# Performance work log

Measured on AMD Instinct MI355X. Metric: run time of the kernel, lower is better.

The kernel has to match this reference:

```python
import jax, jax.numpy as jnp
import numpy as np

B, T, I, H = 64, 2048, 64, 128


def setup_inputs() -> dict:
    key = jax.random.key(0)
    ks = jax.random.split(key, 6)
    std = 1.0 / np.sqrt(H)
    return {
        "x": jax.random.normal(ks[0], (B, T, I), dtype=jnp.float32),
        "h0": jax.random.normal(ks[1], (B, H), dtype=jnp.float32),
        "W": jax.random.uniform(ks[2], (H, I), dtype=jnp.float32, minval=-std, maxval=std),
        "U": jax.random.uniform(ks[3], (H, H), dtype=jnp.float32, minval=-std, maxval=std),
        "b_ih": jax.random.uniform(ks[4], (H,), dtype=jnp.float32, minval=-std, maxval=std),
        "b_hh": jax.random.uniform(ks[5], (H,), dtype=jnp.float32, minval=-std, maxval=std),
    }


def reference(x, h0, W, U, b_ih, b_hh):
    # Precompute the input projection for all timesteps in one big GEMM:
    # xw[b,t,h] = W x_t + b_ih + b_hh  (biases folded in once)
    xw = jnp.einsum("bti,hi->bth", x, W) + b_ih + b_hh  # [B,T,H]
    xw_t = jnp.swapaxes(xw, 0, 1)  # [T,B,H] for scan over time

    def step(h, xt):
        # vanilla tanh RNN cell: h' = tanh(W x + U h + b_ih + b_hh)
        h_new = jnp.tanh(xt + h @ U.T)
        return h_new, h_new

    h_last, ys = jax.lax.scan(step, h0, xw_t)  # ys: [T,B,H]
    output = jnp.swapaxes(ys, 0, 1)  # batch_first -> [B,T,H]
    return output, h_last
```

## Files before the change

### kernel.cpp

```cpp
#include <hip/hip_runtime.h>
#include <hip/hip_bf16.h>


#define RNN_B 64
#define RNN_T 2048
#define RNN_I 64
#define RNN_H 128
#define CH    32
#define NCH   (RNN_T / CH)

__device__ __forceinline__ float fast_tanh(float x) {
  float e = __builtin_amdgcn_exp2f(x * 2.885390081777927f);
  return 1.0f - 2.0f * __builtin_amdgcn_rcpf(e + 1.0f);
}

template <int CTRL>
__device__ __forceinline__ float dpp_add(float s) {
  int o = __builtin_amdgcn_mov_dpp(__float_as_int(s), CTRL, 0xF, 0xF, true);
  return s + __int_as_float(o);
}

__global__ __launch_bounds__(256) void rnn_xw_gemm(
    const float* __restrict__ x, const float* __restrict__ W,
    const float* __restrict__ b_ih, const float* __restrict__ b_hh,
    float* __restrict__ xw) {
  const int tid  = threadIdx.x;
  const int h    = tid >> 1;
  const int half = tid & 1;

  const float4* W4 = (const float4*)(W + h * RNN_I + half * 32);
  float4 w[8];
#pragma unroll
  for (int j = 0; j < 8; ++j) w[j] = W4[j];
  const float bias = b_ih[h] + b_hh[h];

  __shared__ __align__(16) float4 xs[64 * 16];
  const long rbase = (long)blockIdx.x * 64;
  const float4* xg = (const float4*)(x + rbase * RNN_I);
#pragma unroll
  for (int j = 0; j < 4; ++j) xs[tid + 256 * j] = xg[tid + 256 * j];
  __syncthreads();

  for (int r = 0; r < 64; ++r) {
    const float4* xr = xs + r * 16 + half * 8;
    float4 a = make_float4(0.f, 0.f, 0.f, 0.f);
#pragma unroll
    for (int j = 0; j < 8; ++j) {
      float4 xv = xr[j];
      a.x = fmaf(w[j].x, xv.x, a.x);
      a.y = fmaf(w[j].y, xv.y, a.y);
      a.z = fmaf(w[j].z, xv.z, a.z);
      a.w = fmaf(w[j].w, xv.w, a.w);
    }
    float s = (a.x + a.y) + (a.z + a.w);
    s = dpp_add<0xB1>(s);
    if (half == 0)
      xw[(rbase + r) * RNN_H + h] = s + bias;
  }
}

__global__ __launch_bounds__(512, 2) void rnn_scan(
    const float* xw,
    float* out, float* __restrict__ hlast,
    const float* __restrict__ h0, const float* __restrict__ U) {
  const int b   = blockIdx.x;
  const int tid = threadIdx.x;
  const int h   = tid >> 2;
  const int q   = tid & 3;

  __shared__ __align__(16) float hbuf[2][4 * 36];
  __shared__ __align__(16) float xbuf[CH * RNN_H];
  __shared__ __align__(16) float obuf[CH * RNN_H];

  const float4* U4 = (const float4*)(U + h * RNN_H + q * 32);
  float4 u[8];
#pragma unroll
  for (int j = 0; j < 8; ++j) u[j] = U4[j];

  if (tid < RNN_H) hbuf[0][(tid >> 5) * 36 + (tid & 31)] = h0[b * RNN_H + tid];

  const long base    = (long)b * RNN_T * RNN_H;
  const float4* xw4  = (const float4*)(xw + base);
  float4* out4       = (float4*)(out + base);
  float4* xb4        = (float4*)xbuf;
  const float4* ob4  = (const float4*)obuf;

  int cur = 0;
  for (int c = 0; c < NCH; ++c) {
    float4 xr0 = xw4[(long)c * 1024 + tid];
    float4 xr1 = xw4[(long)c * 1024 + tid + 512];
    if (c > 0) {
      float4 o0 = ob4[tid];
      float4 o1 = ob4[tid + 512];
      out4[(long)(c - 1) * 1024 + tid]       = o0;
      out4[(long)(c - 1) * 1024 + tid + 512] = o1;
    }
    xb4[tid]       = xr0;
    xb4[tid + 512] = xr1;
    __syncthreads();

    for (int tc = 0; tc < CH; ++tc) {
      const float4* hp = (const float4*)(hbuf[cur] + q * 36);
      float4 a = make_float4(0.f, 0.f, 0.f, 0.f);
#pragma unroll
      for (int j = 0; j < 8; ++j) {
        float4 hv = hp[j];
        a.x = fmaf(u[j].x, hv.x, a.x);
        a.y = fmaf(u[j].y, hv.y, a.y);
        a.z = fmaf(u[j].z, hv.z, a.z);
        a.w = fmaf(u[j].w, hv.w, a.w);
      }
      float s = (a.x + a.y) + (a.z + a.w);
      s = dpp_add<0xB1>(s);
      s = dpp_add<0x4E>(s);
      float val = fast_tanh(s + xbuf[tc * RNN_H + h]);
      if (q == 0) hbuf[cur ^ 1][(h >> 5) * 36 + (h & 31)] = val;
      if (q == 1) obuf[tc * RNN_H + h] = val;
      cur ^= 1;
      __syncthreads();
    }
  }

  out4[(long)(NCH - 1) * 1024 + tid]       = ob4[tid];
  out4[(long)(NCH - 1) * 1024 + tid + 512] = ob4[tid + 512];
  if (tid < RNN_H)
    hlast[b * RNN_H + tid] = hbuf[cur][(tid >> 5) * 36 + (tid & 31)];
}

extern "C" void kernel_launch(void* const* d_in, const int* in_sizes, int n_in,
                              void* d_out, int out_size, void* d_ws, size_t ws_size,
                              hipStream_t stream) {
  const float* x    = (const float*)d_in[0];
  const float* h0   = (const float*)d_in[1];
  const float* W    = (const float*)d_in[2];
  const float* U    = (const float*)d_in[3];
  const float* b_ih = (const float*)d_in[4];
  const float* b_hh = (const float*)d_in[5];

  float* out   = (float*)d_out;
  float* hlast = out + (long)RNN_B * RNN_T * RNN_H;

  rnn_xw_gemm<<<(RNN_B * RNN_T) / 64, 256, 0, stream>>>(x, W, b_ih, b_hh, out);
  rnn_scan<<<RNN_B, 512, 0, stream>>>(out, out, hlast, h0, U);
}
```

Measured before the change: 771.1 us.

## Register-tile 4 rows per thread in scan and GEMM, halve scan block size

After: 759.6 us. About the same (-1.5%).

```diff
diff --git a/kernel.cpp b/kernel.cpp
--- a/kernel.cpp
+++ b/kernel.cpp
@@ -1,5 +1,4 @@
 #include <hip/hip_runtime.h>
-#include <hip/hip_bf16.h>
 
 
 #define RNN_B 64
@@ -20,111 +19,150 @@
   return s + __int_as_float(o);
 }
 
-__global__ __launch_bounds__(256) void rnn_xw_gemm(
+__device__ __forceinline__ void fma4(float4& a, const float4 u, const float4 h) {
+  a.x = fmaf(u.x, h.x, a.x);
+  a.y = fmaf(u.y, h.y, a.y);
+  a.z = fmaf(u.z, h.z, a.z);
+  a.w = fmaf(u.w, h.w, a.w);
+}
+
+__device__ __forceinline__ float hsum(const float4 a) {
+  return (a.x + a.y) + (a.z + a.w);
+}
+
+__global__ __launch_bounds__(256, 2) void rnn_xw_gemm(
     const float* __restrict__ x, const float* __restrict__ W,
     const float* __restrict__ b_ih, const float* __restrict__ b_hh,
     float* __restrict__ xw) {
-  const int tid  = threadIdx.x;
-  const int h    = tid >> 1;
-  const int half = tid & 1;
+  const int tid   = threadIdx.x;
+  const int wave  = tid >> 6;
+  const int lane  = tid & 63;
+  const int whalf = wave & 1;
+  const int pair  = wave >> 1;
+  const int g2    = lane >> 2;
+  const int q2    = lane & 3;
 
-  const float4* W4 = (const float4*)(W + h * RNN_I + half * 32);
-  float4 w[8];
+  float4 w[4][4];
 #pragma unroll
-  for (int j = 0; j < 8; ++j) w[j] = W4[j];
-  const float bias = b_ih[h] + b_hh[h];
+  for (int r = 0; r < 4; ++r) {
+    const float4* Wr =
+        (const float4*)(W + (64 * whalf + 4 * g2 + r) * RNN_I + 16 * q2);
+#pragma unroll
+    for (int m = 0; m < 4; ++m) w[r][m] = Wr[m];
+  }
+  const int row_own = 64 * whalf + lane;
+  const float bias  = b_ih[row_own] + b_hh[row_own];
 
   __shared__ __align__(16) float4 xs[64 * 16];
   const long rbase = (long)blockIdx.x * 64;
   const float4* xg = (const float4*)(x + rbase * RNN_I);
 #pragma unroll
-  for (int j = 0; j < 4; ++j) xs[tid + 256 * j] = xg[tid + 256 * j];
+  for (int jj = 0; jj < 4; ++jj) xs[tid + 256 * jj] = xg[tid + 256 * jj];
   __syncthreads();
 
-  for (int r = 0; r < 64; ++r) {
-    const float4* xr = xs + r * 16 + half * 8;
-    float4 a = make_float4(0.f, 0.f, 0.f, 0.f);
+  for (int i = 0; i < 32; ++i) {
+    const int r = 32 * pair + i;
+    const float4* xr = xs + r * 16 + q2 * 4;
+    float4 a0 = {0,0,0,0}, a1 = {0,0,0,0}, a2 = {0,0,0,0}, a3 = {0,0,0,0};
 #pragma unroll
-    for (int j = 0; j < 8; ++j) {
-      float4 xv = xr[j];
-      a.x = fmaf(w[j].x, xv.x, a.x);
-      a.y = fmaf(w[j].y, xv.y, a.y);
-      a.z = fmaf(w[j].z, xv.z, a.z);
-      a.w = fmaf(w[j].w, xv.w, a.w);
+    for (int m = 0; m < 4; ++m) {
+      const float4 xv = xr[m];
+      fma4(a0, w[0][m], xv);
+      fma4(a1, w[1][m], xv);
+      fma4(a2, w[2][m], xv);
+      fma4(a3, w[3][m], xv);
     }
-    float s = (a.x + a.y) + (a.z + a.w);
-    s = dpp_add<0xB1>(s);
-    if (half == 0)
-      xw[(rbase + r) * RNN_H + h] = s + bias;
+    float s0 = hsum(a0), s1 = hsum(a1), s2 = hsum(a2), s3 = hsum(a3);
+    s0 = dpp_add<0xB1>(s0); s0 = dpp_add<0x4E>(s0);
+    s1 = dpp_add<0xB1>(s1); s1 = dpp_add<0x4E>(s1);
+    s2 = dpp_add<0xB1>(s2); s2 = dpp_add<0x4E>(s2);
+    s3 = dpp_add<0xB1>(s3); s3 = dpp_add<0x4E>(s3);
+    const float own = (q2 & 2) ? ((q2 & 1) ? s3 : s2)
+                               : ((q2 & 1) ? s1 : s0);
+    xw[(rbase + r) * RNN_H + row_own] = own + bias;
   }
 }
 
-__global__ __launch_bounds__(512, 2) void rnn_scan(
+__global__ __launch_bounds__(256, 1) void rnn_scan(
     const float* xw,
     float* out, float* __restrict__ hlast,
     const float* __restrict__ h0, const float* __restrict__ U) {
-  const int b   = blockIdx.x;
-  const int tid = threadIdx.x;
-  const int h   = tid >> 2;
-  const int q   = tid & 3;
+  const int b     = blockIdx.x;
+  const int tid   = threadIdx.x;
+  const int g     = tid >> 3;
+  const int j     = tid & 7;
+  const int r_own = 4 * g + (j & 3);
 
-  __shared__ __align__(16) float hbuf[2][4 * 36];
+  __shared__ __align__(16) float hbuf0[8 * 20];
+  __shared__ __align__(16) float hbuf1[8 * 20];
   __shared__ __align__(16) float xbuf[CH * RNN_H];
   __shared__ __align__(16) float obuf[CH * RNN_H];
 
-  const float4* U4 = (const float4*)(U + h * RNN_H + q * 32);
-  float4 u[8];
+  float4 u[4][4];
 #pragma unroll
-  for (int j = 0; j < 8; ++j) u[j] = U4[j];
+  for (int r = 0; r < 4; ++r) {
+    const float4* Ur = (const float4*)(U + (4 * g + r) * RNN_H + 16 * j);
+#pragma unroll
+    for (int m = 0; m < 4; ++m) u[r][m] = Ur[m];
+  }
 
-  if (tid < RNN_H) hbuf[0][(tid >> 5) * 36 + (tid & 31)] = h0[b * RNN_H + tid];
+  if (tid < RNN_H)
+    hbuf0[(tid >> 4) * 20 + (tid & 15)] = h0[b * RNN_H + tid];
 
-  const long base    = (long)b * RNN_T * RNN_H;
-  const float4* xw4  = (const float4*)(xw + base);
-  float4* out4       = (float4*)(out + base);
-  float4* xb4        = (float4*)xbuf;
-  const float4* ob4  = (const float4*)obuf;
+  const int hoff = (r_own >> 4) * 20 + (r_own & 15);
+  const long base   = (long)b * RNN_T * RNN_H;
+  const float4* xw4 = (const float4*)(xw + base);
+  float4* out4      = (float4*)(out + base);
+  float4* xb4       = (float4*)xbuf;
+  const float4* ob4 = (const float4*)obuf;
 
-  int cur = 0;
+  auto step = [&](const float* src, float* dst, int tc) {
+    const float xv = xbuf[tc * RNN_H + r_own];
+    const float4* hp = (const float4*)(src + 20 * j);
+    float4 a0 = {0,0,0,0}, a1 = {0,0,0,0}, a2 = {0,0,0,0}, a3 = {0,0,0,0};
+#pragma unroll
+    for (int m = 0; m < 4; ++m) {
+      const float4 hv = hp[m];
+      fma4(a0, u[0][m], hv);
+      fma4(a1, u[1][m], hv);
+      fma4(a2, u[2][m], hv);
+      fma4(a3, u[3][m], hv);
+    }
+    float s0 = hsum(a0), s1 = hsum(a1), s2 = hsum(a2), s3 = hsum(a3);
+    s0 = dpp_add<0xB1>(s0); s0 = dpp_add<0x4E>(s0); s0 = dpp_add<0x141>(s0);
+    s1 = dpp_add<0xB1>(s1); s1 = dpp_add<0x4E>(s1); s1 = dpp_add<0x141>(s1);
+    s2 = dpp_add<0xB1>(s2); s2 = dpp_add<0x4E>(s2); s2 = dpp_add<0x141>(s2);
+    s3 = dpp_add<0xB1>(s3); s3 = dpp_add<0x4E>(s3); s3 = dpp_add<0x141>(s3);
+    const float own = (j & 2) ? ((j & 1) ? s3 : s2)
+                              : ((j & 1) ? s1 : s0);
+    const float val = fast_tanh(own + xv);
+    float* wp = (j < 4) ? (dst + hoff) : (obuf + tc * RNN_H + r_own);
+    *wp = val;
+    __syncthreads();
+  };
+
   for (int c = 0; c < NCH; ++c) {
-    float4 xr0 = xw4[(long)c * 1024 + tid];
-    float4 xr1 = xw4[(long)c * 1024 + tid + 512];
+#pragma unroll
+    for (int jj = 0; jj < 4; ++jj)
+      xb4[tid + 256 * jj] = xw4[(long)c * 1024 + tid + 256 * jj];
     if (c > 0) {
-      float4 o0 = ob4[tid];
-      float4 o1 = ob4[tid + 512];
-      out4[(long)(c - 1) * 1024 + tid]       = o0;
-      out4[(long)(c - 1) * 1024 + tid + 512] = o1;
+#pragma unroll
+      for (int jj = 0; jj < 4; ++jj)
+        out4[(long)(c - 1) * 1024 + tid + 256 * jj] = ob4[tid + 256 * jj];
     }
-    xb4[tid]       = xr0;
-    xb4[tid + 512] = xr1;
     __syncthreads();
 
-    for (int tc = 0; tc < CH; ++tc) {
-      const float4* hp = (const float4*)(hbuf[cur] + q * 36);
-      float4 a = make_float4(0.f, 0.f, 0.f, 0.f);
-#pragma unroll
-      for (int j = 0; j < 8; ++j) {
-        float4 hv = hp[j];
-        a.x = fmaf(u[j].x, hv.x, a.x);
-        a.y = fmaf(u[j].y, hv.y, a.y);
-        a.z = fmaf(u[j].z, hv.z, a.z);
-        a.w = fmaf(u[j].w, hv.w, a.w);
-      }
-      float s = (a.x + a.y) + (a.z + a.w);
-      s = dpp_add<0xB1>(s);
-      s = dpp_add<0x4E>(s);
-      float val = fast_tanh(s + xbuf[tc * RNN_H + h]);
-      if (q == 0) hbuf[cur ^ 1][(h >> 5) * 36 + (h & 31)] = val;
-      if (q == 1) obuf[tc * RNN_H + h] = val;
-      cur ^= 1;
-      __syncthreads();
+    for (int tc = 0; tc < CH; tc += 2) {
+      step(hbuf0, hbuf1, tc);
+      step(hbuf1, hbuf0, tc + 1);
     }
   }
 
-  out4[(long)(NCH - 1) * 1024 + tid]       = ob4[tid];
-  out4[(long)(NCH - 1) * 1024 + tid + 512] = ob4[tid + 512];
+#pragma unroll
+  for (int jj = 0; jj < 4; ++jj)
+    out4[(long)(NCH - 1) * 1024 + tid + 256 * jj] = ob4[tid + 256 * jj];
   if (tid < RNN_H)
-    hlast[b * RNN_H + tid] = hbuf[cur][(tid >> 5) * 36 + (tid & 31)];
+    hlast[b * RNN_H + tid] = hbuf0[(tid >> 4) * 20 + (tid & 15)];
 }
 
 extern "C" void kernel_launch(void* const* d_in, const int* in_sizes, int n_in,
@@ -141,5 +179,5 @@
   float* hlast = out + (long)RNN_B * RNN_T * RNN_H;
 
   rnn_xw_gemm<<<(RNN_B * RNN_T) / 64, 256, 0, stream>>>(x, W, b_ih, b_hh, out);
-  rnn_scan<<<RNN_B, 512, 0, stream>>>(out, out, hlast, h0, U);
+  rnn_scan<<<RNN_B, 256, 0, stream>>>(out, out, hlast, h0, U);
 }
```
